# Kernel optimization log

Hardware: AMD Instinct MI355X
Metric: run time of the kernel (lower is better)

## Reference

```python
import jax, jax.numpy as jnp
import numpy as np

DIM_Z, DIM_X, DIM_S = 64, 32, 16
T, N_SIMS = 1024, 1024


def _softplus_eps(x, eps=1e-6):
    return jax.nn.softplus(x) + eps


def setup_inputs() -> dict:
    key = jax.random.key(0)
    ks = jax.random.split(key, 9)
    r_z = 1.0 / np.sqrt(DIM_Z)
    r_s = 1.0 / np.sqrt(DIM_S)
    return {
        "u": jax.random.normal(ks[0], (T, N_SIMS, DIM_S), jnp.float32),
        "z0": jax.random.normal(ks[1], (N_SIMS, DIM_Z), jnp.float32),
        "noise_z": jax.random.normal(ks[2], (T, N_SIMS, DIM_Z), jnp.float32),
        "noise_x": jax.random.normal(ks[3], (T, N_SIMS, DIM_X), jnp.float32),
        "AW": jax.random.uniform(ks[4], (DIM_Z, DIM_Z), jnp.float32, -r_z, r_z),
        "C": jax.random.uniform(ks[5], (DIM_Z, DIM_S), jnp.float32, -r_s, r_s),
        "B": jax.random.uniform(ks[6], (DIM_X, DIM_Z), jnp.float32, -r_z, r_z),
        "Q": jax.random.uniform(ks[7], (DIM_Z,), jnp.float32, -0.01, 0.01),
        "R": jax.random.uniform(ks[8], (DIM_X,), jnp.float32, -0.01, 0.01),
    }


def reference(u, z0, noise_z, noise_x, AW, C, B, Q, R):
    """PF_PLRNN.simulate: T-step latent PLRNN rollout with Gaussian noise.

    z_{t+1} = A_diag*z_t + relu(z_t) @ W_off.T + u_t @ C.T + eps_z * q
    x_t     = z_t @ B.T + eps_x * r
    Returns z: (T, n_sims, d), x: (T, n_sims, p).
    """
    A_diag = jnp.diag(AW)            # (d,)
    W_off = AW - jnp.diag(A_diag)    # zero-diagonal off-part
    q = _softplus_eps(Q)             # (d,) process noise std
    r = _softplus_eps(R)             # (p,) emission noise std

    def step(z_t, inp):
        u_t, nz, nx = inp
        x_t = z_t @ B.T + nx * r                                  # (n, p)
        mu = z_t * A_diag + jax.nn.relu(z_t) @ W_off.T + u_t @ C.T  # (n, d)
        z_next = mu + nz * q
        return z_next, (z_t, x_t)

    _, (z, x) = jax.lax.scan(step, z0, (u, noise_z, noise_x))
    return z, x
```

## Files before the change

### kernel.cpp

```cpp
#include <hip/hip_runtime.h>

#define DZ 64
#define DX 32
#define DS 16
#define TT 1024
#define NS 1024
#define SNZ (NS * DZ)
#define SNX (NS * DX)
#define SU4 (NS * DS / 4)

#define AW_B 0
#define C_B  (AW_B + DZ * (DZ + 1))
#define B_B  (C_B + DZ * (DS + 1))
#define SMEM_FLOATS (B_B + DX * (DZ + 1))
#define ZR_O 0
#define RZ_O DZ
#define PM_O (2 * DZ)
#define PX_O (2 * DZ + 256)

__device__ __forceinline__ float softplus_eps(float x) {
    return fmaxf(x, 0.f) + log1pf(expf(-fabsf(x))) + 1e-6f;
}

__global__ __launch_bounds__(128, 2) void plrnn_split_kernel(
    const float* __restrict__ u,
    const float* __restrict__ z0,
    const float* __restrict__ nz,
    const float* __restrict__ nx,
    const float* __restrict__ AW,
    const float* __restrict__ Cm,
    const float* __restrict__ Bm,
    const float* __restrict__ Q,
    const float* __restrict__ R,
    float* __restrict__ zo,
    float* __restrict__ xo)
{
    const int tid  = threadIdx.x;
    const int lane = tid & 63;
    const int kh   = tid >> 6;
    const int p    = lane & 31;
    const int sim  = __builtin_amdgcn_readfirstlane((int)blockIdx.x);

    __shared__ float smem[SMEM_FLOATS];

    {
        const int r = tid >> 1;
        const int c = (tid & 1) * 32;
        #pragma unroll
        for (int k = 0; k < 32; ++k) smem[AW_B + r * (DZ + 1) + c + k] = AW[r * DZ + c + k];
        const int cc = (tid & 1) * 8;
        #pragma unroll
        for (int k = 0; k < 8; ++k) smem[C_B + r * (DS + 1) + cc + k] = Cm[r * DS + cc + k];
        const int br = tid >> 2;
        const int bc = (tid & 3) * 16;
        #pragma unroll
        for (int k = 0; k < 16; ++k) smem[B_B + br * (DZ + 1) + bc + k] = Bm[br * DZ + bc + k];
    }
    __syncthreads();

    float Wrow[32];
    #pragma unroll
    for (int j = 0; j < 32; ++j) {
        const int k = 32 * kh + j;
        const float w = smem[AW_B + lane * (DZ + 1) + k];
        Wrow[j] = (k == lane) ? 0.f : w;
    }
    const float Ad = smem[AW_B + lane * (DZ + 1) + lane];
    float Crow[8];
    #pragma unroll
    for (int j = 0; j < 8; ++j) Crow[j] = smem[C_B + lane * (DS + 1) + 8 * kh + j];
    const int kq = 32 * kh + ((lane >> 5) << 4);
    float Brow[16];
    #pragma unroll
    for (int j = 0; j < 16; ++j) Brow[j] = smem[B_B + p * (DZ + 1) + kq + j];

    const float qv = softplus_eps(Q[lane]);
    const float rv = softplus_eps(R[p]);

    __syncthreads();

    float zl = z0[sim * DZ + lane];

    const float*  nzb = nz + sim * DZ;
    const float*  nxb = nx + sim * DX;
    const float4* ub4 = (const float4*)(u + sim * DS + 8 * kh);
    float* zob = zo + sim * DZ;
    float* xob = xo + sim * DX;

    float nzp[4], nxp[4];
    float4 upA[4], upB[4];
    #pragma unroll
    for (int j = 0; j < 4; ++j) {
        nzp[j] = nzb[lane + j * SNZ];
        nxp[j] = nxb[p + j * SNX];
        upA[j] = ub4[j * SU4];
        upB[j] = ub4[j * SU4 + 1];
    }

    for (int t0 = 0; t0 < TT; t0 += 4) {
        #pragma unroll
        for (int j = 0; j < 4; ++j) {
            const int t   = t0 + j;
            const int par = j & 1;
            const float  vnz = nzp[j];
            const float  vnx = nxp[j];
            const float4 ua  = upA[j];
            const float4 ubv = upB[j];

            smem[ZR_O + lane] = zl;
            smem[RZ_O + lane] = fmaxf(zl, 0.f);
            if (kh == 0) zob[lane + t * SNZ] = zl;

            float m0 = Crow[0] * ua.x,  m1 = Crow[1] * ua.y;
            float m2 = Crow[2] * ua.z,  m3 = Crow[3] * ua.w;
            m0 = fmaf(Crow[4], ubv.x, m0); m1 = fmaf(Crow[5], ubv.y, m1);
            m2 = fmaf(Crow[6], ubv.z, m2); m3 = fmaf(Crow[7], ubv.w, m3);

            {
                int tn = t + 4; tn = (tn < TT) ? tn : (TT - 1);
                nzp[j] = nzb[lane + tn * SNZ];
                nxp[j] = nxb[p + tn * SNX];
                upA[j] = ub4[tn * SU4];
                upB[j] = ub4[tn * SU4 + 1];
            }

            #pragma unroll
            for (int k4 = 0; k4 < 8; ++k4) {
                const float4 zz = *(const float4*)&smem[RZ_O + 32 * kh + 4 * k4];
                m0 = fmaf(Wrow[4 * k4 + 0], zz.x, m0);
                m1 = fmaf(Wrow[4 * k4 + 1], zz.y, m1);
                m2 = fmaf(Wrow[4 * k4 + 2], zz.z, m2);
                m3 = fmaf(Wrow[4 * k4 + 3], zz.w, m3);
            }

            float xa0 = 0.f, xa1 = 0.f;
            #pragma unroll
            for (int k4 = 0; k4 < 4; ++k4) {
                const float4 zz = *(const float4*)&smem[ZR_O + kq + 4 * k4];
                xa0 = fmaf(Brow[4 * k4 + 0], zz.x, xa0);
                xa1 = fmaf(Brow[4 * k4 + 1], zz.y, xa1);
                xa0 = fmaf(Brow[4 * k4 + 2], zz.z, xa0);
                xa1 = fmaf(Brow[4 * k4 + 3], zz.w, xa1);
            }
            float xpart = xa0 + xa1;
            xpart += __shfl_xor(xpart, 32);

            const float mown = (m0 + m1) + (m2 + m3);
            smem[PM_O + par * 128 + kh * 64 + lane] = mown;
            if (kh == 0 && lane < 32) smem[PX_O + par * 32 + p] = xpart;

            __syncthreads();

            const float moth = smem[PM_O + par * 128 + (1 - kh) * 64 + lane];
            const float h0 = (kh == 0) ? mown : moth;
            const float h1 = (kh == 0) ? moth : mown;

            if (kh == 1 && lane < 32) {
                const float xoth = smem[PX_O + par * 32 + p];
                xob[p + t * SNX] = fmaf(vnx, rv, xpart + xoth);
            }

            zl = fmaf(qv, vnz, fmaf(Ad, zl, h0 + h1));
        }
    }
}

extern "C" void kernel_launch(void* const* d_in, const int* in_sizes, int n_in,
                              void* d_out, int out_size, void* d_ws, size_t ws_size,
                              hipStream_t stream) {
    const float* u_  = (const float*)d_in[0];
    const float* z0_ = (const float*)d_in[1];
    const float* nz_ = (const float*)d_in[2];
    const float* nx_ = (const float*)d_in[3];
    const float* AW_ = (const float*)d_in[4];
    const float* C_  = (const float*)d_in[5];
    const float* B_  = (const float*)d_in[6];
    const float* Q_  = (const float*)d_in[7];
    const float* R_  = (const float*)d_in[8];

    float* zo = (float*)d_out;
    float* xo = zo + (size_t)TT * NS * DZ;

    hipLaunchKernelGGL(plrnn_split_kernel, dim3(NS), dim3(128), 0, stream,
                       u_, z0_, nz_, nx_, AW_, C_, B_, Q_, R_, zo, xo);
}
```

Baseline: 456.8 us.

## Split each simulation's recurrence across four wavefronts with chunked weight staging

Measured after the change: 800.2 us. +75.2%, slower.

```diff
diff --git a/kernel.cpp b/kernel.cpp
--- a/kernel.cpp
+++ b/kernel.cpp
@@ -7,22 +7,19 @@
 #define NS 1024
 #define SNZ (NS * DZ)
 #define SNX (NS * DX)
-#define SU4 (NS * DS / 4)
-
-#define AW_B 0
-#define C_B  (AW_B + DZ * (DZ + 1))
-#define B_B  (C_B + DZ * (DS + 1))
-#define SMEM_FLOATS (B_B + DX * (DZ + 1))
+#define SU  (NS * DS)
+
 #define ZR_O 0
-#define RZ_O DZ
-#define PM_O (2 * DZ)
-#define PX_O (2 * DZ + 256)
+#define RZ_O 64
+#define PM_O 128
+#define PX_O 640
+#define SMEM_FLOATS 896
 
 __device__ __forceinline__ float softplus_eps(float x) {
     return fmaxf(x, 0.f) + log1pf(expf(-fabsf(x))) + 1e-6f;
 }
 
-__global__ __launch_bounds__(128, 2) void plrnn_split_kernel(
+__global__ __launch_bounds__(256, 4) void plrnn_q_kernel(
     const float* __restrict__ u,
     const float* __restrict__ z0,
     const float* __restrict__ nz,
@@ -37,42 +34,62 @@
 {
     const int tid  = threadIdx.x;
     const int lane = tid & 63;
-    const int kh   = tid >> 6;
+    const int wvu  = __builtin_amdgcn_readfirstlane(tid >> 6);
     const int p    = lane & 31;
+    const int h    = lane >> 5;
+    const int kx   = 16 * wvu + 8 * h;
     const int sim  = __builtin_amdgcn_readfirstlane((int)blockIdx.x);
 
     __shared__ float smem[SMEM_FLOATS];
 
-    {
-        const int r = tid >> 1;
-        const int c = (tid & 1) * 32;
-        #pragma unroll
-        for (int k = 0; k < 32; ++k) smem[AW_B + r * (DZ + 1) + c + k] = AW[r * DZ + c + k];
-        const int cc = (tid & 1) * 8;
-        #pragma unroll
-        for (int k = 0; k < 8; ++k) smem[C_B + r * (DS + 1) + cc + k] = Cm[r * DS + cc + k];
-        const int br = tid >> 2;
-        const int bc = (tid & 3) * 16;
-        #pragma unroll
-        for (int k = 0; k < 16; ++k) smem[B_B + br * (DZ + 1) + bc + k] = Bm[br * DZ + bc + k];
-    }
-    __syncthreads();
-
-    float Wrow[32];
-    #pragma unroll
-    for (int j = 0; j < 32; ++j) {
-        const int k = 32 * kh + j;
-        const float w = smem[AW_B + lane * (DZ + 1) + k];
-        Wrow[j] = (k == lane) ? 0.f : w;
-    }
-    const float Ad = smem[AW_B + lane * (DZ + 1) + lane];
-    float Crow[8];
-    #pragma unroll
-    for (int j = 0; j < 8; ++j) Crow[j] = smem[C_B + lane * (DS + 1) + 8 * kh + j];
-    const int kq = 32 * kh + ((lane >> 5) << 4);
-    float Brow[16];
-    #pragma unroll
-    for (int j = 0; j < 16; ++j) Brow[j] = smem[B_B + p * (DZ + 1) + kq + j];
+    float Wrow[16];
+    float Ad = 0.f;
+    for (int ch = 0; ch < 8; ++ch) {
+        __syncthreads();
+        for (int i = tid; i < 520; i += 256) {
+            const int rr = i / 65, cc = i - rr * 65;
+            if (cc < 64) smem[i] = AW[(ch * 8 + rr) * 64 + cc];
+        }
+        __syncthreads();
+        if ((lane >> 3) == ch) {
+            const int r = lane & 7;
+            #pragma unroll
+            for (int j2 = 0; j2 < 16; ++j2) {
+                const int k = 16 * wvu + j2;
+                const float w = smem[r * 65 + k];
+                Wrow[j2] = (k == lane) ? 0.f : w;
+            }
+            Ad = smem[r * 65 + lane];
+        }
+    }
+    float Crow[4];
+    for (int ch = 0; ch < 2; ++ch) {
+        __syncthreads();
+        for (int i = tid; i < 544; i += 256) {
+            const int rr = i / 17, cc = i - rr * 17;
+            if (cc < 16) smem[i] = Cm[(ch * 32 + rr) * 16 + cc];
+        }
+        __syncthreads();
+        if ((lane >> 5) == ch) {
+            const int r = lane & 31;
+            #pragma unroll
+            for (int j2 = 0; j2 < 4; ++j2) Crow[j2] = smem[r * 17 + 4 * wvu + j2];
+        }
+    }
+    float Brow[8];
+    for (int ch = 0; ch < 4; ++ch) {
+        __syncthreads();
+        for (int i = tid; i < 520; i += 256) {
+            const int rr = i / 65, cc = i - rr * 65;
+            if (cc < 64) smem[i] = Bm[(ch * 8 + rr) * 64 + cc];
+        }
+        __syncthreads();
+        if ((p >> 3) == ch) {
+            const int r = p & 7;
+            #pragma unroll
+            for (int j2 = 0; j2 < 8; ++j2) Brow[j2] = smem[r * 65 + kx + j2];
+        }
+    }
 
     const float qv = softplus_eps(Q[lane]);
     const float rv = softplus_eps(R[p]);
@@ -81,20 +98,19 @@
 
     float zl = z0[sim * DZ + lane];
 
-    const float*  nzb = nz + sim * DZ;
-    const float*  nxb = nx + sim * DX;
-    const float4* ub4 = (const float4*)(u + sim * DS + 8 * kh);
+    const float* nzb = nz + sim * DZ;
+    const float* nxb = nx + sim * DX;
+    const float* ub  = u  + sim * DS + 4 * wvu;
     float* zob = zo + sim * DZ;
     float* xob = xo + sim * DX;
 
     float nzp[4], nxp[4];
-    float4 upA[4], upB[4];
+    float4 uqp[4];
     #pragma unroll
     for (int j = 0; j < 4; ++j) {
         nzp[j] = nzb[lane + j * SNZ];
         nxp[j] = nxb[p + j * SNX];
-        upA[j] = ub4[j * SU4];
-        upB[j] = ub4[j * SU4 + 1];
+        uqp[j] = *(const float4*)(ub + j * SU);
     }
 
     for (int t0 = 0; t0 < TT; t0 += 4) {
@@ -104,63 +120,62 @@
             const int par = j & 1;
             const float  vnz = nzp[j];
             const float  vnx = nxp[j];
-            const float4 ua  = upA[j];
-            const float4 ubv = upB[j];
+            const float4 uq  = uqp[j];
 
             smem[ZR_O + lane] = zl;
             smem[RZ_O + lane] = fmaxf(zl, 0.f);
-            if (kh == 0) zob[lane + t * SNZ] = zl;
-
-            float m0 = Crow[0] * ua.x,  m1 = Crow[1] * ua.y;
-            float m2 = Crow[2] * ua.z,  m3 = Crow[3] * ua.w;
-            m0 = fmaf(Crow[4], ubv.x, m0); m1 = fmaf(Crow[5], ubv.y, m1);
-            m2 = fmaf(Crow[6], ubv.z, m2); m3 = fmaf(Crow[7], ubv.w, m3);
+            if (wvu == 0) zob[lane + t * SNZ] = zl;
+
+            float m0 = Crow[0] * uq.x, m1 = Crow[1] * uq.y;
+            float m2 = Crow[2] * uq.z, m3 = Crow[3] * uq.w;
 
             {
                 int tn = t + 4; tn = (tn < TT) ? tn : (TT - 1);
                 nzp[j] = nzb[lane + tn * SNZ];
                 nxp[j] = nxb[p + tn * SNX];
-                upA[j] = ub4[tn * SU4];
-                upB[j] = ub4[tn * SU4 + 1];
-            }
-
-            #pragma unroll
-            for (int k4 = 0; k4 < 8; ++k4) {
-                const float4 zz = *(const float4*)&smem[RZ_O + 32 * kh + 4 * k4];
+                uqp[j] = *(const float4*)(ub + tn * SU);
+            }
+
+            #pragma unroll
+            for (int k4 = 0; k4 < 4; ++k4) {
+                const float4 zz = *(const float4*)&smem[RZ_O + 16 * wvu + 4 * k4];
                 m0 = fmaf(Wrow[4 * k4 + 0], zz.x, m0);
                 m1 = fmaf(Wrow[4 * k4 + 1], zz.y, m1);
                 m2 = fmaf(Wrow[4 * k4 + 2], zz.z, m2);
                 m3 = fmaf(Wrow[4 * k4 + 3], zz.w, m3);
             }
 
-            float xa0 = 0.f, xa1 = 0.f;
-            #pragma unroll
-            for (int k4 = 0; k4 < 4; ++k4) {
-                const float4 zz = *(const float4*)&smem[ZR_O + kq + 4 * k4];
-                xa0 = fmaf(Brow[4 * k4 + 0], zz.x, xa0);
-                xa1 = fmaf(Brow[4 * k4 + 1], zz.y, xa1);
-                xa0 = fmaf(Brow[4 * k4 + 2], zz.z, xa0);
-                xa1 = fmaf(Brow[4 * k4 + 3], zz.w, xa1);
+            float xa0, xa1;
+            {
+                const float4 za = *(const float4*)&smem[ZR_O + kx];
+                const float4 zb = *(const float4*)&smem[ZR_O + kx + 4];
+                xa0 = Brow[0] * za.x;            xa1 = Brow[1] * za.y;
+                xa0 = fmaf(Brow[2], za.z, xa0);  xa1 = fmaf(Brow[3], za.w, xa1);
+                xa0 = fmaf(Brow[4], zb.x, xa0);  xa1 = fmaf(Brow[5], zb.y, xa1);
+                xa0 = fmaf(Brow[6], zb.z, xa0);  xa1 = fmaf(Brow[7], zb.w, xa1);
             }
             float xpart = xa0 + xa1;
             xpart += __shfl_xor(xpart, 32);
 
-            const float mown = (m0 + m1) + (m2 + m3);
-            smem[PM_O + par * 128 + kh * 64 + lane] = mown;
-            if (kh == 0 && lane < 32) smem[PX_O + par * 32 + p] = xpart;
+            smem[PM_O + par * 256 + wvu * 64 + lane] = (m0 + m1) + (m2 + m3);
+            if (lane < 32) smem[PX_O + par * 128 + wvu * 32 + p] = xpart;
 
             __syncthreads();
 
-            const float moth = smem[PM_O + par * 128 + (1 - kh) * 64 + lane];
-            const float h0 = (kh == 0) ? mown : moth;
-            const float h1 = (kh == 0) ? moth : mown;
-
-            if (kh == 1 && lane < 32) {
-                const float xoth = smem[PX_O + par * 32 + p];
-                xob[p + t * SNX] = fmaf(vnx, rv, xpart + xoth);
-            }
-
-            zl = fmaf(qv, vnz, fmaf(Ad, zl, h0 + h1));
+            const float q0 = smem[PM_O + par * 256 +   0 + lane];
+            const float q1 = smem[PM_O + par * 256 +  64 + lane];
+            const float q2 = smem[PM_O + par * 256 + 128 + lane];
+            const float q3 = smem[PM_O + par * 256 + 192 + lane];
+
+            if (wvu == 3 && lane < 32) {
+                const float xs = (smem[PX_O + par * 128 +  0 + p]
+                                + smem[PX_O + par * 128 + 32 + p])
+                               + (smem[PX_O + par * 128 + 64 + p]
+                                + smem[PX_O + par * 128 + 96 + p]);
+                xob[p + t * SNX] = fmaf(vnx, rv, xs);
+            }
+
+            zl = fmaf(qv, vnz, fmaf(Ad, zl, (q0 + q1) + (q2 + q3)));
         }
     }
 }
@@ -181,6 +196,6 @@
     float* zo = (float*)d_out;
     float* xo = zo + (size_t)TT * NS * DZ;
 
-    hipLaunchKernelGGL(plrnn_split_kernel, dim3(NS), dim3(128), 0, stream,
+    hipLaunchKernelGGL(plrnn_q_kernel, dim3(NS), dim3(256), 0, stream,
                        u_, z0_, nz_, nx_, AW_, C_, B_, Q_, R_, zo, xo);
 }
```
